# Kernel optimization log

Measured on AMD Instinct MI355X. Metric: run time of the kernel, lower is better.

The kernel has to match this reference:

```python
import jax, jax.numpy as jnp
import numpy as np

B, N, D, K, H = 32768, 17, 2, 3, 64


def _mlp_params(key, n, d_in, d_hid, d_out):
    k1, k2, k3, k4 = jax.random.split(key, 4)
    W1 = jax.random.normal(k1, (n, d_in, d_hid), jnp.float32) / np.sqrt(d_in)
    b1 = jnp.zeros((n, d_hid), jnp.float32)
    W2 = jax.random.normal(k2, (n, d_hid, d_out), jnp.float32) / np.sqrt(d_hid)
    b2 = jnp.zeros((n, d_out), jnp.float32)
    return W1, b1, W2, b2


def setup_inputs() -> dict:
    key = jax.random.key(0)
    kp, kk, kw, kb = jax.random.split(key, 4)
    pred_pts = jax.random.normal(kp, (B, N, D), jnp.float32)
    kW1, kb1, kW2, kb2 = _mlp_params(kk, N, D, H, K)            # k_nets
    wW1, wb1, wW2, wb2 = _mlp_params(kw, N, D, H, K)            # weight_nets
    bW1, bb1, bW2, bb2 = _mlp_params(kb, N, D, 2 * H, K * 2 * D)  # basis_nets
    return dict(pred_pts=pred_pts,
                kW1=kW1, kb1=kb1, kW2=kW2, kb2=kb2,
                wW1=wW1, wb1=wb1, wW2=wW2, wb2=wb2,
                bW1=bW1, bb1=bb1, bW2=bW2, bb2=bb2)


def _per_joint_mlp(x, W1, b1, W2, b2):
    # x: [B,N,D]; W1: [N,D,Hd]; W2: [N,Hd,O]
    h = jax.nn.relu(jnp.einsum('bnd,ndh->bnh', x, W1) + b1[None])
    return jnp.einsum('bnh,nho->bno', h, W2) + b2[None]


def reference(pred_pts, kW1, kb1, kW2, kb2, wW1, wb1, wW2, wb2, bW1, bb1, bW2, bb2):
    Bc, Nc, Dc = pred_pts.shape
    Kc = kW2.shape[-1]

    # k-selection head (eval mode: argmax, +1)
    k_logits = _per_joint_mlp(pred_pts, kW1, kb1, kW2, kb2)      # [B,N,K]
    k_js = jnp.argmax(k_logits, axis=-1) + 1                     # [B,N] int

    # mixture weights
    w = jax.nn.softmax(_per_joint_mlp(pred_pts, wW1, wb1, wW2, wb2), axis=-1)  # [B,N,K]

    # basis parameters: mu, sigma = exp(log_sigma)
    params = _per_joint_mlp(pred_pts, bW1, bb1, bW2, bb2).reshape(Bc, Nc, Kc, 2 * Dc)
    mu = params[..., :Dc]                                         # [B,N,K,D]
    sigma = jnp.exp(params[..., Dc:])                             # [B,N,K,D]

    # top-k selection by descending weight (indices are constants w.r.t. grad)
    idx = jnp.argsort(-w, axis=-1)                                # [B,N,K]
    mu_top = jnp.take_along_axis(mu, idx[..., None], axis=2)      # [B,N,K,D]
    sigma_top = jnp.take_along_axis(sigma, idx[..., None], axis=2)
    mask = jnp.arange(Kc)[None, None, :] < k_js[..., None]        # [B,N,K] bool

    # pack float outputs: weights + selected (mu, sigma) -> [B,N,K,1+2D]
    out = jnp.concatenate([w[..., None], mu_top, sigma_top], axis=-1)
    return out, k_js, mask
```

## Files before the change

kernel.cpp:

```cpp
#include <hip/hip_runtime.h>
#include <cmath>

#define NBATCH 32768
#define NJOINT 17
#define OUT0_ELEMS (NBATCH * NJOINT * 15)
#define KJS_OFF    OUT0_ELEMS
#define MASK_OFF   (KJS_OFF + NBATCH * NJOINT)

#define WN_STRIDE 774
#define WS_DOUBLES (NJOINT * WN_STRIDE)

#define BW_FLT 2064

__device__ __forceinline__ float sel3f(int i, float a, float b, float c) {
    return (i == 0) ? a : ((i == 1) ? b : c);
}

__global__ void cvt_weights_f64(
    const float* __restrict__ kW1, const float* __restrict__ kb1,
    const float* __restrict__ kW2, const float* __restrict__ kb2,
    const float* __restrict__ wW1, const float* __restrict__ wb1,
    const float* __restrict__ wW2, const float* __restrict__ wb2,
    double* __restrict__ dws)
{
    const int n = blockIdx.x;
    double* o = dws + (size_t)n * WN_STRIDE;
    for (int i = threadIdx.x; i < WN_STRIDE; i += blockDim.x) {
        int j = i;
        const float* W1 = kW1; const float* b1 = kb1;
        const float* W2 = kW2; const float* b2 = kb2;
        if (j >= 387) { j -= 387; W1 = wW1; b1 = wb1; W2 = wW2; b2 = wb2; }
        float v;
        if (j < 128)      v = W1[n * 128 + j];
        else if (j < 192) v = b1[n * 64 + (j - 128)];
        else if (j < 384) v = W2[n * 192 + (j - 192)];
        else              v = b2[n * 3 + (j - 384)];
        o[i] = (double)v;
    }
}

__device__ __forceinline__ void mlp32_2(
    const float* __restrict__ W1, const float* __restrict__ b1f,
    const float* __restrict__ W2f, const float* __restrict__ b2f, int n,
    float xA0, float xA1, float xB0, float xB1,
    float& lA0, float& lA1, float& lA2,
    float& lB0, float& lB1, float& lB2)
{
    const float* W1a = W1 + n * 128;
    const float* W1b = W1a + 64;
    const float* b1  = b1f + n * 64;
    const float* W2  = W2f + n * 192;
    lA0 = b2f[n * 3 + 0]; lB0 = lA0;
    lA1 = b2f[n * 3 + 1]; lB1 = lA1;
    lA2 = b2f[n * 3 + 2]; lB2 = lA2;
    #pragma unroll 4
    for (int h = 0; h < 64; ++h) {
        const float wa = W1a[h], wb = W1b[h], bb = b1[h];
        const float w0 = W2[h * 3 + 0], w1 = W2[h * 3 + 1], w2 = W2[h * 3 + 2];
        float hvA = fmaxf(fmaf(xA1, wb, fmaf(xA0, wa, bb)), 0.0f);
        float hvB = fmaxf(fmaf(xB1, wb, fmaf(xB0, wa, bb)), 0.0f);
        lA0 = fmaf(hvA, w0, lA0); lB0 = fmaf(hvB, w0, lB0);
        lA1 = fmaf(hvA, w1, lA1); lB1 = fmaf(hvB, w1, lB1);
        lA2 = fmaf(hvA, w2, lA2); lB2 = fmaf(hvB, w2, lB2);
    }
}

__device__ __forceinline__ void mlp64_ws_1(
    const double* __restrict__ gws, double x0, double x1,
    double& l0, double& l1, double& l2)
{
    const double* W1a = gws;
    const double* W1b = gws + 64;
    const double* b1  = gws + 128;
    const double* W2  = gws + 192;
    l0 = gws[384]; l1 = gws[385]; l2 = gws[386];
    #pragma unroll 4
    for (int h = 0; h < 64; ++h) {
        double hv = fmax(fma(x1, W1b[h], fma(x0, W1a[h], b1[h])), 0.0);
        l0 = fma(hv, W2[h * 3 + 0], l0);
        l1 = fma(hv, W2[h * 3 + 1], l1);
        l2 = fma(hv, W2[h * 3 + 2], l2);
    }
}

__device__ __forceinline__ void mlp64_cvt_1(
    const float* __restrict__ W1, const float* __restrict__ b1f,
    const float* __restrict__ W2f, const float* __restrict__ b2f, int n,
    double x0, double x1, double& l0, double& l1, double& l2)
{
    const float* W1a = W1 + n * 128;
    const float* W1b = W1a + 64;
    const float* b1  = b1f + n * 64;
    const float* W2  = W2f + n * 192;
    l0 = (double)b2f[n * 3 + 0];
    l1 = (double)b2f[n * 3 + 1];
    l2 = (double)b2f[n * 3 + 2];
    #pragma unroll 4
    for (int h = 0; h < 64; ++h) {
        double hv = fma(x1, (double)W1b[h], fma(x0, (double)W1a[h], (double)b1[h]));
        hv = fmax(hv, 0.0);
        l0 = fma(hv, (double)W2[h * 3 + 0], l0);
        l1 = fma(hv, (double)W2[h * 3 + 1], l1);
        l2 = fma(hv, (double)W2[h * 3 + 2], l2);
    }
}

__device__ __forceinline__ bool tight3(float a, float b, float c) {
    const float m01 = fabsf(a - b), m02 = fabsf(a - c), m12 = fabsf(b - c);
    const float mn = fminf(m01, fminf(m02, m12));
    const float tau = 1e-3f * (1.0f + 0.02f * (fabsf(a) + fabsf(b) + fabsf(c)));
    return mn < tau;
}

__device__ __forceinline__ void decide(
    double kl0, double kl1, double kl2,
    double wl0, double wl1, double wl2,
    int& kj, int& i0, int& i1, int& i2,
    float& p0, float& p1, float& p2)
{
    kj = 0;
    {
        double m = kl0;
        if (kl1 > m) { m = kl1; kj = 1; }
        if (kl2 > m) { kj = 2; }
    }
    i0 = 0;
    {
        double m = wl0;
        if (wl1 > m) { m = wl1; i0 = 1; }
        if (wl2 > m) { i0 = 2; }
    }
    const int ia = (i0 == 0) ? 1 : 0;
    const int ib = (i0 == 2) ? 1 : 2;
    const double wa = ia ? wl1 : wl0;
    const double wb = (ib == 1) ? wl1 : wl2;
    i1 = (wb > wa) ? ib : ia;
    i2 = (wb > wa) ? ia : ib;

    const double mw = fmax(fmax(wl0, wl1), wl2);
    const float e0 = __expf((float)(wl0 - mw));
    const float e1 = __expf((float)(wl1 - mw));
    const float e2 = __expf((float)(wl2 - mw));
    const float inv = 1.0f / (e0 + e1 + e2);
    p0 = e0 * inv; p1 = e1 * inv; p2 = e2 * inv;
}

__device__ __forceinline__ void epilogue(
    const float acc[12], int i0, int i1, int i2,
    float p0, float p1, float p2, float r[15])
{
    r[0]  = p0; r[5] = p1; r[10] = p2;
    r[1]  = sel3f(i0, acc[0], acc[4], acc[8]);
    r[2]  = sel3f(i0, acc[1], acc[5], acc[9]);
    r[3]  = __expf(sel3f(i0, acc[2], acc[6], acc[10]));
    r[4]  = __expf(sel3f(i0, acc[3], acc[7], acc[11]));
    r[6]  = sel3f(i1, acc[0], acc[4], acc[8]);
    r[7]  = sel3f(i1, acc[1], acc[5], acc[9]);
    r[8]  = __expf(sel3f(i1, acc[2], acc[6], acc[10]));
    r[9]  = __expf(sel3f(i1, acc[3], acc[7], acc[11]));
    r[11] = sel3f(i2, acc[0], acc[4], acc[8]);
    r[12] = sel3f(i2, acc[1], acc[5], acc[9]);
    r[13] = __expf(sel3f(i2, acc[2], acc[6], acc[10]));
    r[14] = __expf(sel3f(i2, acc[3], acc[7], acc[11]));
}

__device__ __forceinline__ void store_point(
    float* __restrict__ out, int p, const float r[15], int kj)
{
    float* o = out + (size_t)p * 15;
    #pragma unroll
    for (int i = 0; i < 15; ++i) o[i] = r[i];
    out[KJS_OFF + p] = (float)(kj + 1);
    float* mk = out + MASK_OFF + (size_t)p * 3;
    mk[0] = 1.0f;
    mk[1] = (kj >= 1) ? 1.0f : 0.0f;
    mk[2] = (kj >= 2) ? 1.0f : 0.0f;
}

template<bool USE_WS>
__global__ __launch_bounds__(256, 4) void mdn_fused(
    const float* __restrict__ pred_pts,
    const float* __restrict__ kW1, const float* __restrict__ kb1,
    const float* __restrict__ kW2, const float* __restrict__ kb2,
    const float* __restrict__ wW1, const float* __restrict__ wb1,
    const float* __restrict__ wW2, const float* __restrict__ wb2,
    const float* __restrict__ bW1, const float* __restrict__ bb1,
    const float* __restrict__ bW2, const float* __restrict__ bb2,
    float* __restrict__ out,
    const double* __restrict__ dws)
{
    const int tid = threadIdx.x;
    const int bid = blockIdx.x;
    const int n   = bid >> 6;
    const int bxx = bid & 63;

    __shared__ __align__(16) float bw[BW_FLT];
    for (int j = tid; j < BW_FLT; j += 256) {
        const int g = j >> 4, s = j & 15;
        float f;
        if (g < 128) {
            f = (s == 0) ? bW1[n * 256 + g]
              : (s == 1) ? bW1[n * 256 + 128 + g]
              : (s == 2) ? bb1[n * 128 + g]
              : (s == 3) ? 0.0f
              :            bW2[n * 1536 + g * 12 + (s - 4)];
        } else {
            f = (s < 12) ? bb2[n * 12 + s] : 0.0f;
        }
        bw[j] = f;
    }

    const int bA = bxx * 512 + tid;
    const int bB = bA + 256;
    const int pA = bA * NJOINT + n;
    const int pB = bB * NJOINT + n;
    const float2 xA = *reinterpret_cast<const float2*>(pred_pts + 2 * pA);
    const float2 xB = *reinterpret_cast<const float2*>(pred_pts + 2 * pB);

    __syncthreads();

    float kA0, kA1, kA2, kB0, kB1, kB2;
    float wA0, wA1, wA2, wB0, wB1, wB2;
    mlp32_2(kW1, kb1, kW2, kb2, n, xA.x, xA.y, xB.x, xB.y,
            kA0, kA1, kA2, kB0, kB1, kB2);
    mlp32_2(wW1, wb1, wW2, wb2, n, xA.x, xA.y, xB.x, xB.y,
            wA0, wA1, wA2, wB0, wB1, wB2);

    const bool fA = tight3(kA0, kA1, kA2) || tight3(wA0, wA1, wA2);
    const bool fB = tight3(kB0, kB1, kB2) || tight3(wB0, wB1, wB2);

    double klA0 = kA0, klA1 = kA1, klA2 = kA2;
    double klB0 = kB0, klB1 = kB1, klB2 = kB2;
    double wlA0 = wA0, wlA1 = wA1, wlA2 = wA2;
    double wlB0 = wB0, wlB1 = wB1, wlB2 = wB2;

    if (__any(fA || fB)) {
        if constexpr (USE_WS) {
            const double* Wn = dws + (size_t)n * WN_STRIDE;
            if (fA) {
                mlp64_ws_1(Wn,       (double)xA.x, (double)xA.y, klA0, klA1, klA2);
                mlp64_ws_1(Wn + 387, (double)xA.x, (double)xA.y, wlA0, wlA1, wlA2);
            }
            if (fB) {
                mlp64_ws_1(Wn,       (double)xB.x, (double)xB.y, klB0, klB1, klB2);
                mlp64_ws_1(Wn + 387, (double)xB.x, (double)xB.y, wlB0, wlB1, wlB2);
            }
        } else {
            if (fA) {
                mlp64_cvt_1(kW1, kb1, kW2, kb2, n, (double)xA.x, (double)xA.y, klA0, klA1, klA2);
                mlp64_cvt_1(wW1, wb1, wW2, wb2, n, (double)xA.x, (double)xA.y, wlA0, wlA1, wlA2);
            }
            if (fB) {
                mlp64_cvt_1(kW1, kb1, kW2, kb2, n, (double)xB.x, (double)xB.y, klB0, klB1, klB2);
                mlp64_cvt_1(wW1, wb1, wW2, wb2, n, (double)xB.x, (double)xB.y, wlB0, wlB1, wlB2);
            }
        }
    }

    int kjA, i0A, i1A, i2A, kjB, i0B, i1B, i2B;
    float p0A, p1A, p2A, p0B, p1B, p2B;
    decide(klA0, klA1, klA2, wlA0, wlA1, wlA2, kjA, i0A, i1A, i2A, p0A, p1A, p2A);
    decide(klB0, klB1, klB2, wlB0, wlB1, wlB2, kjB, i0B, i1B, i2B, p0B, p1B, p2B);

    float accA[12], accB[12];
    #pragma unroll
    for (int j = 0; j < 12; ++j) { const float t = bw[2048 + j]; accA[j] = t; accB[j] = t; }
    #pragma unroll 4
    for (int h = 0; h < 128; ++h) {
        const float4* g4 = reinterpret_cast<const float4*>(bw + (h << 4));
        const float4 q0 = g4[0], q1 = g4[1], q2 = g4[2], q3 = g4[3];
        const float hvA = fmaxf(fmaf(xA.y, q0.y, fmaf(xA.x, q0.x, q0.z)), 0.0f);
        const float hvB = fmaxf(fmaf(xB.y, q0.y, fmaf(xB.x, q0.x, q0.z)), 0.0f);
        accA[0]  = fmaf(hvA, q1.x, accA[0]);  accB[0]  = fmaf(hvB, q1.x, accB[0]);
        accA[1]  = fmaf(hvA, q1.y, accA[1]);  accB[1]  = fmaf(hvB, q1.y, accB[1]);
        accA[2]  = fmaf(hvA, q1.z, accA[2]);  accB[2]  = fmaf(hvB, q1.z, accB[2]);
        accA[3]  = fmaf(hvA, q1.w, accA[3]);  accB[3]  = fmaf(hvB, q1.w, accB[3]);
        accA[4]  = fmaf(hvA, q2.x, accA[4]);  accB[4]  = fmaf(hvB, q2.x, accB[4]);
        accA[5]  = fmaf(hvA, q2.y, accA[5]);  accB[5]  = fmaf(hvB, q2.y, accB[5]);
        accA[6]  = fmaf(hvA, q2.z, accA[6]);  accB[6]  = fmaf(hvB, q2.z, accB[6]);
        accA[7]  = fmaf(hvA, q2.w, accA[7]);  accB[7]  = fmaf(hvB, q2.w, accB[7]);
        accA[8]  = fmaf(hvA, q3.x, accA[8]);  accB[8]  = fmaf(hvB, q3.x, accB[8]);
        accA[9]  = fmaf(hvA, q3.y, accA[9]);  accB[9]  = fmaf(hvB, q3.y, accB[9]);
        accA[10] = fmaf(hvA, q3.z, accA[10]); accB[10] = fmaf(hvB, q3.z, accB[10]);
        accA[11] = fmaf(hvA, q3.w, accA[11]); accB[11] = fmaf(hvB, q3.w, accB[11]);
    }

    float rA[15], rB[15];
    epilogue(accA, i0A, i1A, i2A, p0A, p1A, p2A, rA);
    epilogue(accB, i0B, i1B, i2B, p0B, p1B, p2B, rB);

    store_point(out, pA, rA, kjA);
    store_point(out, pB, rB, kjB);
}

extern "C" void kernel_launch(void* const* d_in, const int* in_sizes, int n_in,
                              void* d_out, int out_size, void* d_ws, size_t ws_size,
                              hipStream_t stream) {
    (void)in_sizes; (void)n_in; (void)out_size;
    const bool use_ws = (d_ws != nullptr) && (ws_size >= (size_t)WS_DOUBLES * sizeof(double));
    dim3 grid(NJOINT * 64);
    if (use_ws) {
        cvt_weights_f64<<<NJOINT, 256, 0, stream>>>(
            (const float*)d_in[1], (const float*)d_in[2],
            (const float*)d_in[3], (const float*)d_in[4],
            (const float*)d_in[5], (const float*)d_in[6],
            (const float*)d_in[7], (const float*)d_in[8],
            (double*)d_ws);
        mdn_fused<true><<<grid, 256, 0, stream>>>(
            (const float*)d_in[0],
            (const float*)d_in[1], (const float*)d_in[2],
            (const float*)d_in[3], (const float*)d_in[4],
            (const float*)d_in[5], (const float*)d_in[6],
            (const float*)d_in[7], (const float*)d_in[8],
            (const float*)d_in[9], (const float*)d_in[10],
            (const float*)d_in[11], (const float*)d_in[12],
            (float*)d_out, (const double*)d_ws);
    } else {
        mdn_fused<false><<<grid, 256, 0, stream>>>(
            (const float*)d_in[0],
            (const float*)d_in[1], (const float*)d_in[2],
            (const float*)d_in[3], (const float*)d_in[4],
            (const float*)d_in[5], (const float*)d_in[6],
            (const float*)d_in[7], (const float*)d_in[8],
            (const float*)d_in[9], (const float*)d_in[10],
            (const float*)d_in[11], (const float*)d_in[12],
            (float*)d_out, nullptr);
    }
}
```

Baseline: 165.5 us.

## Restructure into per-joint persistent 1024-thread blocks and tighten fp64 fallback threshold

Launches one 1024-thread block per (joint, batch chunk) with a strided loop over batch elements, processing one point per thread and reading basis-net weights directly from global memory instead of staging them in shared memory. The near-tie threshold that triggers the double-precision recomputation of the selection and weight heads is made much tighter, so fewer waves take the slow fp64 path. This trades the earlier two-points-per-thread register reuse and LDS staging for uniform scalar weight loads and fewer blocks, and the tighter threshold risks argmax/argsort mismatches on near ties.

```diff
diff --git a/kernel.cpp b/kernel.cpp
--- a/kernel.cpp
+++ b/kernel.cpp
@@ -10,7 +10,8 @@
 #define WN_STRIDE 774
 #define WS_DOUBLES (NJOINT * WN_STRIDE)
 
-#define BW_FLT 2064
+#define NCHUNK 15
+#define CHUNKB 2185
 
 __device__ __forceinline__ float sel3f(int i, float a, float b, float c) {
     return (i == 0) ? a : ((i == 1) ? b : c);
@@ -39,29 +40,26 @@
     }
 }
 
-__device__ __forceinline__ void mlp32_2(
+__device__ __forceinline__ void mlp32_1(
     const float* __restrict__ W1, const float* __restrict__ b1f,
     const float* __restrict__ W2f, const float* __restrict__ b2f, int n,
-    float xA0, float xA1, float xB0, float xB1,
-    float& lA0, float& lA1, float& lA2,
-    float& lB0, float& lB1, float& lB2)
+    float x0, float x1, float& l0, float& l1, float& l2)
 {
     const float* W1a = W1 + n * 128;
     const float* W1b = W1a + 64;
     const float* b1  = b1f + n * 64;
     const float* W2  = W2f + n * 192;
-    lA0 = b2f[n * 3 + 0]; lB0 = lA0;
-    lA1 = b2f[n * 3 + 1]; lB1 = lA1;
-    lA2 = b2f[n * 3 + 2]; lB2 = lA2;
+    l0 = b2f[n * 3 + 0];
+    l1 = b2f[n * 3 + 1];
+    l2 = b2f[n * 3 + 2];
     #pragma unroll 4
     for (int h = 0; h < 64; ++h) {
         const float wa = W1a[h], wb = W1b[h], bb = b1[h];
         const float w0 = W2[h * 3 + 0], w1 = W2[h * 3 + 1], w2 = W2[h * 3 + 2];
-        float hvA = fmaxf(fmaf(xA1, wb, fmaf(xA0, wa, bb)), 0.0f);
-        float hvB = fmaxf(fmaf(xB1, wb, fmaf(xB0, wa, bb)), 0.0f);
-        lA0 = fmaf(hvA, w0, lA0); lB0 = fmaf(hvB, w0, lB0);
-        lA1 = fmaf(hvA, w1, lA1); lB1 = fmaf(hvB, w1, lB1);
-        lA2 = fmaf(hvA, w2, lA2); lB2 = fmaf(hvB, w2, lB2);
+        float hv = fmaxf(fmaf(x1, wb, fmaf(x0, wa, bb)), 0.0f);
+        l0 = fmaf(hv, w0, l0);
+        l1 = fmaf(hv, w1, l1);
+        l2 = fmaf(hv, w2, l2);
     }
 }
 
@@ -108,7 +106,7 @@
 __device__ __forceinline__ bool tight3(float a, float b, float c) {
     const float m01 = fabsf(a - b), m02 = fabsf(a - c), m12 = fabsf(b - c);
     const float mn = fminf(m01, fminf(m02, m12));
-    const float tau = 1e-3f * (1.0f + 0.02f * (fabsf(a) + fabsf(b) + fabsf(c)));
+    const float tau = 2e-5f * (1.0f + 0.05f * (fabsf(a) + fabsf(b) + fabsf(c)));
     return mn < tau;
 }
 
@@ -178,7 +176,7 @@
 }
 
 template<bool USE_WS>
-__global__ __launch_bounds__(256, 4) void mdn_fused(
+__global__ __launch_bounds__(1024, 4) void mdn_fused(
     const float* __restrict__ pred_pts,
     const float* __restrict__ kW1, const float* __restrict__ kb1,
     const float* __restrict__ kW2, const float* __restrict__ kb2,
@@ -189,108 +187,69 @@
     float* __restrict__ out,
     const double* __restrict__ dws)
 {
-    const int tid = threadIdx.x;
-    const int bid = blockIdx.x;
-    const int n   = bid >> 6;
-    const int bxx = bid & 63;
-
-    __shared__ __align__(16) float bw[BW_FLT];
-    for (int j = tid; j < BW_FLT; j += 256) {
-        const int g = j >> 4, s = j & 15;
-        float f;
-        if (g < 128) {
-            f = (s == 0) ? bW1[n * 256 + g]
-              : (s == 1) ? bW1[n * 256 + 128 + g]
-              : (s == 2) ? bb1[n * 128 + g]
-              : (s == 3) ? 0.0f
-              :            bW2[n * 1536 + g * 12 + (s - 4)];
-        } else {
-            f = (s < 12) ? bb2[n * 12 + s] : 0.0f;
-        }
-        bw[j] = f;
-    }
-
-    const int bA = bxx * 512 + tid;
-    const int bB = bA + 256;
-    const int pA = bA * NJOINT + n;
-    const int pB = bB * NJOINT + n;
-    const float2 xA = *reinterpret_cast<const float2*>(pred_pts + 2 * pA);
-    const float2 xB = *reinterpret_cast<const float2*>(pred_pts + 2 * pB);
-
-    __syncthreads();
-
-    float kA0, kA1, kA2, kB0, kB1, kB2;
-    float wA0, wA1, wA2, wB0, wB1, wB2;
-    mlp32_2(kW1, kb1, kW2, kb2, n, xA.x, xA.y, xB.x, xB.y,
-            kA0, kA1, kA2, kB0, kB1, kB2);
-    mlp32_2(wW1, wb1, wW2, wb2, n, xA.x, xA.y, xB.x, xB.y,
-            wA0, wA1, wA2, wB0, wB1, wB2);
-
-    const bool fA = tight3(kA0, kA1, kA2) || tight3(wA0, wA1, wA2);
-    const bool fB = tight3(kB0, kB1, kB2) || tight3(wB0, wB1, wB2);
-
-    double klA0 = kA0, klA1 = kA1, klA2 = kA2;
-    double klB0 = kB0, klB1 = kB1, klB2 = kB2;
-    double wlA0 = wA0, wlA1 = wA1, wlA2 = wA2;
-    double wlB0 = wB0, wlB1 = wB1, wlB2 = wB2;
-
-    if (__any(fA || fB)) {
-        if constexpr (USE_WS) {
-            const double* Wn = dws + (size_t)n * WN_STRIDE;
-            if (fA) {
-                mlp64_ws_1(Wn,       (double)xA.x, (double)xA.y, klA0, klA1, klA2);
-                mlp64_ws_1(Wn + 387, (double)xA.x, (double)xA.y, wlA0, wlA1, wlA2);
-            }
-            if (fB) {
-                mlp64_ws_1(Wn,       (double)xB.x, (double)xB.y, klB0, klB1, klB2);
-                mlp64_ws_1(Wn + 387, (double)xB.x, (double)xB.y, wlB0, wlB1, wlB2);
-            }
-        } else {
-            if (fA) {
-                mlp64_cvt_1(kW1, kb1, kW2, kb2, n, (double)xA.x, (double)xA.y, klA0, klA1, klA2);
-                mlp64_cvt_1(wW1, wb1, wW2, wb2, n, (double)xA.x, (double)xA.y, wlA0, wlA1, wlA2);
-            }
-            if (fB) {
-                mlp64_cvt_1(kW1, kb1, kW2, kb2, n, (double)xB.x, (double)xB.y, klB0, klB1, klB2);
-                mlp64_cvt_1(wW1, wb1, wW2, wb2, n, (double)xB.x, (double)xB.y, wlB0, wlB1, wlB2);
+    const int tid   = threadIdx.x;
+    const int bid   = blockIdx.x;
+    const int n     = bid / NCHUNK;
+    const int chunk = bid - n * NCHUNK;
+    const int base  = chunk * CHUNKB;
+    const int bend  = min(base + CHUNKB, NBATCH);
+
+    for (int b = base + tid; b < bend; b += 1024) {
+        const int p = b * NJOINT + n;
+        const float2 xv = *reinterpret_cast<const float2*>(pred_pts + 2 * p);
+        const float x0 = xv.x, x1 = xv.y;
+
+        float kl0f, kl1f, kl2f, wl0f, wl1f, wl2f;
+        mlp32_1(kW1, kb1, kW2, kb2, n, x0, x1, kl0f, kl1f, kl2f);
+        mlp32_1(wW1, wb1, wW2, wb2, n, x0, x1, wl0f, wl1f, wl2f);
+
+        const bool fl = tight3(kl0f, kl1f, kl2f) || tight3(wl0f, wl1f, wl2f);
+
+        double kl0 = kl0f, kl1 = kl1f, kl2 = kl2f;
+        double wl0 = wl0f, wl1 = wl1f, wl2 = wl2f;
+
+        if (__any(fl)) {
+            if constexpr (USE_WS) {
+                const double* Wn = dws + (size_t)n * WN_STRIDE;
+                if (fl) {
+                    mlp64_ws_1(Wn,       (double)x0, (double)x1, kl0, kl1, kl2);
+                    mlp64_ws_1(Wn + 387, (double)x0, (double)x1, wl0, wl1, wl2);
+                }
+            } else {
+                if (fl) {
+                    mlp64_cvt_1(kW1, kb1, kW2, kb2, n, (double)x0, (double)x1, kl0, kl1, kl2);
+                    mlp64_cvt_1(wW1, wb1, wW2, wb2, n, (double)x0, (double)x1, wl0, wl1, wl2);
+                }
             }
         }
-    }
-
-    int kjA, i0A, i1A, i2A, kjB, i0B, i1B, i2B;
-    float p0A, p1A, p2A, p0B, p1B, p2B;
-    decide(klA0, klA1, klA2, wlA0, wlA1, wlA2, kjA, i0A, i1A, i2A, p0A, p1A, p2A);
-    decide(klB0, klB1, klB2, wlB0, wlB1, wlB2, kjB, i0B, i1B, i2B, p0B, p1B, p2B);
-
-    float accA[12], accB[12];
-    #pragma unroll
-    for (int j = 0; j < 12; ++j) { const float t = bw[2048 + j]; accA[j] = t; accB[j] = t; }
-    #pragma unroll 4
-    for (int h = 0; h < 128; ++h) {
-        const float4* g4 = reinterpret_cast<const float4*>(bw + (h << 4));
-        const float4 q0 = g4[0], q1 = g4[1], q2 = g4[2], q3 = g4[3];
-        const float hvA = fmaxf(fmaf(xA.y, q0.y, fmaf(xA.x, q0.x, q0.z)), 0.0f);
-        const float hvB = fmaxf(fmaf(xB.y, q0.y, fmaf(xB.x, q0.x, q0.z)), 0.0f);
-        accA[0]  = fmaf(hvA, q1.x, accA[0]);  accB[0]  = fmaf(hvB, q1.x, accB[0]);
-        accA[1]  = fmaf(hvA, q1.y, accA[1]);  accB[1]  = fmaf(hvB, q1.y, accB[1]);
-        accA[2]  = fmaf(hvA, q1.z, accA[2]);  accB[2]  = fmaf(hvB, q1.z, accB[2]);
-        accA[3]  = fmaf(hvA, q1.w, accA[3]);  accB[3]  = fmaf(hvB, q1.w, accB[3]);
-        accA[4]  = fmaf(hvA, q2.x, accA[4]);  accB[4]  = fmaf(hvB, q2.x, accB[4]);
-        accA[5]  = fmaf(hvA, q2.y, accA[5]);  accB[5]  = fmaf(hvB, q2.y, accB[5]);
-        accA[6]  = fmaf(hvA, q2.z, accA[6]);  accB[6]  = fmaf(hvB, q2.z, accB[6]);
-        accA[7]  = fmaf(hvA, q2.w, accA[7]);  accB[7]  = fmaf(hvB, q2.w, accB[7]);
-        accA[8]  = fmaf(hvA, q3.x, accA[8]);  accB[8]  = fmaf(hvB, q3.x, accB[8]);
-        accA[9]  = fmaf(hvA, q3.y, accA[9]);  accB[9]  = fmaf(hvB, q3.y, accB[9]);
-        accA[10] = fmaf(hvA, q3.z, accA[10]); accB[10] = fmaf(hvB, q3.z, accB[10]);
-        accA[11] = fmaf(hvA, q3.w, accA[11]); accB[11] = fmaf(hvB, q3.w, accB[11]);
-    }
-
-    float rA[15], rB[15];
-    epilogue(accA, i0A, i1A, i2A, p0A, p1A, p2A, rA);
-    epilogue(accB, i0B, i1B, i2B, p0B, p1B, p2B, rB);
-
-    store_point(out, pA, rA, kjA);
-    store_point(out, pB, rB, kjB);
+
+        int kj, i0, i1, i2;
+        float p0, p1, p2;
+        decide(kl0, kl1, kl2, wl0, wl1, wl2, kj, i0, i1, i2, p0, p1, p2);
+
+        float acc[12];
+        {
+            const float* W1a = bW1 + n * 256;
+            const float* W1b = W1a + 128;
+            const float* b1  = bb1 + n * 128;
+            const float* W2  = bW2 + n * 1536;
+            const float* b2  = bb2 + n * 12;
+            #pragma unroll
+            for (int j = 0; j < 12; ++j) acc[j] = b2[j];
+            #pragma unroll 4
+            for (int h = 0; h < 128; ++h) {
+                const float wa = W1a[h], wb = W1b[h], bb = b1[h];
+                float hv = fmaxf(fmaf(x1, wb, fmaf(x0, wa, bb)), 0.0f);
+                #pragma unroll
+                for (int j = 0; j < 12; ++j)
+                    acc[j] = fmaf(hv, W2[h * 12 + j], acc[j]);
+            }
+        }
+
+        float r[15];
+        epilogue(acc, i0, i1, i2, p0, p1, p2, r);
+        store_point(out, p, r, kj);
+    }
 }
 
 extern "C" void kernel_launch(void* const* d_in, const int* in_sizes, int n_in,
@@ -298,7 +257,7 @@
                               hipStream_t stream) {
     (void)in_sizes; (void)n_in; (void)out_size;
     const bool use_ws = (d_ws != nullptr) && (ws_size >= (size_t)WS_DOUBLES * sizeof(double));
-    dim3 grid(NJOINT * 64);
+    dim3 grid(NJOINT * NCHUNK);
     if (use_ws) {
         cvt_weights_f64<<<NJOINT, 256, 0, stream>>>(
             (const float*)d_in[1], (const float*)d_in[2],
@@ -306,7 +265,7 @@
             (const float*)d_in[5], (const float*)d_in[6],
             (const float*)d_in[7], (const float*)d_in[8],
             (double*)d_ws);
-        mdn_fused<true><<<grid, 256, 0, stream>>>(
+        mdn_fused<true><<<grid, 1024, 0, stream>>>(
             (const float*)d_in[0],
             (const float*)d_in[1], (const float*)d_in[2],
             (const float*)d_in[3], (const float*)d_in[4],
@@ -316,7 +275,7 @@
             (const float*)d_in[11], (const float*)d_in[12],
             (float*)d_out, (const double*)d_ws);
     } else {
-        mdn_fused<false><<<grid, 256, 0, stream>>>(
+        mdn_fused<false><<<grid, 1024, 0, stream>>>(
             (const float*)d_in[0],
             (const float*)d_in[1], (const float*)d_in[2],
             (const float*)d_in[3], (const float*)d_in[4],
```

After: 166.8 us. Within noise of the previous version (+0.7%).
